# Kernel tuning notes

Measured on AMD Instinct MI355X. Metric: run time of the kernel, lower is better.

Reference implementation:

```python
import jax, jax.numpy as jnp
import numpy as np

B, N, L, H, D, IN = 512, 128, 10, 16, 8, 16
NT = B * N
E = NT * 16

def _lin(key, fan_in, shape):
    b = 1.0 / np.sqrt(fan_in)
    return jax.random.uniform(key, shape, jnp.float32, -b, b)

def setup_inputs() -> dict:
    key = jax.random.key(0)
    ks = jax.random.split(key, 12)
    x = jax.random.normal(ks[0], (NT, IN), jnp.float32)
    # within-graph random edges so to_dense_adj is well defined
    g = jax.random.randint(ks[1], (E,), 0, B)
    i = jax.random.randint(ks[2], (E,), 0, N)
    j = jax.random.randint(ks[3], (E,), 0, N)
    edge_index = jnp.stack([g * N + i, g * N + j]).astype(jnp.int32)
    return dict(
        x=x,
        gin_w1=_lin(ks[4], H, (2, L, H, H)),   # [ld/ud, layer, H, H]
        gin_b1=_lin(ks[5], H, (2, L, H)),
        gin_w2=_lin(ks[6], H, (2, L, H, H)),
        gin_b2=_lin(ks[7], H, (2, L, H)),
        mean_w=_lin(ks[8], H, (2, H, D)),
        mean_b=jnp.zeros((2, D), jnp.float32),
        std_w=_lin(ks[9], H, (2, H, D)),
        std_b=jnp.zeros((2, D), jnp.float32),
        edge_index=edge_index,
    )

def _encoder(x, w1, b1, w2, b2, mw, mb, sw, sb, src, dst):
    # PyG GIN stack: GINConv(MLP[Lin->ReLU->Lin]), eps=0, sum aggregation,
    # ReLU between layers (dropout = identity in eval mode).
    h = x
    for l in range(L):
        agg = jax.ops.segment_sum(h[src], dst, num_segments=NT)
        t = h + agg  # (1+eps)*x + sum_{j in N(i)} x_j with eps=0
        t = jnp.maximum(t @ w1[l] + b1[l], 0.0) @ w2[l] + b2[l]
        h = jnp.maximum(t, 0.0) if l < L - 1 else t
    mean = h @ mw + mb
    std = jax.nn.softplus(h @ sw + sb)
    return mean, std

def reference(x, gin_w1, gin_b1, gin_w2, gin_b2, mean_w, mean_b, std_w, std_b, edge_index):
    src, dst = edge_index[0], edge_index[1]
    enc = jax.vmap(_encoder, in_axes=(None, 0, 0, 0, 0, 0, 0, 0, 0, None, None))
    mean, std = enc(x, gin_w1, gin_b1, gin_w2, gin_b2,
                    mean_w, mean_b, std_w, std_b, src, dst)  # [2, NT, D]
    # reparameterized sample: eps ~ N(0,1) (prior.sample, detached)
    eps = jax.random.normal(jax.random.key(42), (2, NT, D), jnp.float32)
    z = mean + std * eps
    z_ld = z[0].reshape(B, N, D)
    z_ud = z[1].reshape(B, N, D)
    logits = jnp.einsum('bnd,bmd->bnm', z_ld, z_ud)  # per-graph inner-product decode
    dense_adj = jnp.zeros((B, N, N), jnp.float32).at[src // N, src % N, dst % N].add(1.0)
    n_pos = dense_adj.sum()
    posw = (B * N * N - n_pos) / n_pos
    # BCE-with-logits, pos_weight, reduction='sum'
    nll = jnp.sum(posw * dense_adj * jax.nn.softplus(-logits)
                  + (1.0 - dense_adj) * jax.nn.softplus(logits))
    # KL(N(mean,std) || N(0,1)), summed over both encoders
    kl = jnp.sum(-jnp.log(std) + 0.5 * (std * std + mean * mean) - 0.5)
    return nll, kl, jax.nn.sigmoid(logits), dense_adj
```

## Files before the change

kernel.cpp:

```cpp
#include <hip/hip_runtime.h>

#define B_    512
#define N_    128
#define L_    10
#define H_    16
#define D_    8
#define NT_   65536
#define E_    1048576
#define NNB_  8388608
#define CAP_  4096
#define CCAP_ 2816
#define HS_   20
#define PLANE_ (129*HS_ + 4)

__device__ __forceinline__ unsigned rotl32(unsigned v, int r){ return (v<<r)|(v>>(32-r)); }

__device__ __forceinline__ void threefry2x32(unsigned c0, unsigned c1, unsigned &o0, unsigned &o1){
  const unsigned ks0 = 0u, ks1 = 42u, ks2 = 0u ^ 42u ^ 0x1BD11BDAu;
  unsigned x0 = c0 + ks0, x1 = c1 + ks1;
#define TFR(r) { x0 += x1; x1 = rotl32(x1, r); x1 ^= x0; }
  TFR(13) TFR(15) TFR(26) TFR(6)   x0 += ks1; x1 += ks2 + 1u;
  TFR(17) TFR(29) TFR(16) TFR(24)  x0 += ks2; x1 += ks0 + 2u;
  TFR(13) TFR(15) TFR(26) TFR(6)   x0 += ks0; x1 += ks1 + 3u;
  TFR(17) TFR(29) TFR(16) TFR(24)  x0 += ks1; x1 += ks2 + 4u;
  TFR(13) TFR(15) TFR(26) TFR(6)   x0 += ks2; x1 += ks0 + 5u;
#undef TFR
  o0 = x0; o1 = x1;
}

__device__ __forceinline__ float erfinv_f(float x){
  float w = -log1pf(-x*x);
  float p;
  if (w < 5.0f) {
    w -= 2.5f;
    p = 2.81022636e-08f;
    p = fmaf(p, w, 3.43273939e-07f);
    p = fmaf(p, w, -3.5233877e-06f);
    p = fmaf(p, w, -4.39150654e-06f);
    p = fmaf(p, w, 0.00021858087f);
    p = fmaf(p, w, -0.00125372503f);
    p = fmaf(p, w, -0.00417768164f);
    p = fmaf(p, w, 0.246640727f);
    p = fmaf(p, w, 1.50140941f);
  } else {
    w = sqrtf(w) - 3.0f;
    p = -0.000200214257f;
    p = fmaf(p, w, 0.000100950558f);
    p = fmaf(p, w, 0.00134934322f);
    p = fmaf(p, w, -0.00367342844f);
    p = fmaf(p, w, 0.00573950773f);
    p = fmaf(p, w, -0.0076224613f);
    p = fmaf(p, w, 0.00943887047f);
    p = fmaf(p, w, 1.00167406f);
    p = fmaf(p, w, 2.83297682f);
  }
  return p * x;
}

__device__ __forceinline__ float softplus_f(float x){
  return fmaxf(x, 0.0f) + log1pf(expf(-fabsf(x)));
}

__device__ __forceinline__ void blockReduceAdd(double v, double* target){
  __shared__ double red[16];
  int lane = threadIdx.x & 63;
  int w    = threadIdx.x >> 6;
  #pragma unroll
  for(int off = 32; off > 0; off >>= 1) v += __shfl_down(v, off);
  if(lane == 0) red[w] = v;
  __syncthreads();
  if(threadIdx.x == 0){
    double s = red[0];
    int nw = (blockDim.x + 63) >> 6;
    for(int k = 1; k < nw; k++) s += red[k];
    atomicAdd(target, s);
  }
}

__device__ __forceinline__ float clamp_finite(double v){
  if(v != v) return 0.0f;
  if(v >  3.3e38) return  3.3e38f;
  if(v < -3.3e38) return -3.3e38f;
  return (float)v;
}

__global__ __launch_bounds__(1024)
void k_bin(const int* __restrict__ ei, int* __restrict__ gcount,
           unsigned short* __restrict__ ebuf){
  __shared__ int skv[4096];
  __shared__ int cnt[512];
  __shared__ int gb[512];
  __shared__ int off[512];
  __shared__ int wtot[8];
  const int t = threadIdx.x;
  if(t < 512) cnt[t] = 0;
  __syncthreads();
  int kv[4];
  const int base = blockIdx.x * 4096;
  #pragma unroll
  for(int k = 0; k < 4; k++){
    int e = base + k*1024 + t;
    int s = ei[e];
    int d = ei[E_ + e];
    int g = d >> 7;
    kv[k] = (g << 14) | ((s & 127) << 7) | (d & 127);
    atomicAdd(&cnt[g], 1);
  }
  __syncthreads();
  int intra = 0;
  if(t < 512){
    int lane = t & 63;
    int myc = cnt[t];
    int s = myc;
    #pragma unroll
    for(int o = 1; o < 64; o <<= 1){
      int v = __shfl_up(s, o);
      if(lane >= o) s += v;
    }
    intra = s - myc;
    if(lane == 63) wtot[t >> 6] = s;
    gb[t] = myc ? atomicAdd(&gcount[t], myc) : 0;
  }
  __syncthreads();
  if(t < 8){
    int v = wtot[t];
    int s = v;
    #pragma unroll
    for(int o = 1; o < 8; o <<= 1){
      int u = __shfl_up(s, o);
      if(t >= o) s += u;
    }
    wtot[t] = s - v;
  }
  if(t < 512) cnt[t] = 0;
  __syncthreads();
  if(t < 512) off[t] = intra + wtot[t >> 6];
  __syncthreads();
  #pragma unroll
  for(int k = 0; k < 4; k++){
    int g = kv[k] >> 14;
    int pos = atomicAdd(&cnt[g], 1);
    skv[off[g] + pos] = kv[k];
  }
  __syncthreads();
  #pragma unroll
  for(int k = 0; k < 4; k++){
    int i = k*1024 + t;
    int v = skv[i];
    int g = v >> 14;
    int idx = gb[g] + (i - off[g]);
    if(idx < CAP_) ebuf[(size_t)g*CAP_ + idx] = (unsigned short)(v & 0x3FFF);
  }
}

__global__ __launch_bounds__(1024, 8)
void k_mega(const float* __restrict__ x, const unsigned short* __restrict__ ebuf,
            const int* __restrict__ gcount,
            const float* __restrict__ gw1, const float* __restrict__ gb1,
            const float* __restrict__ gw2, const float* __restrict__ gb2,
            const float* __restrict__ mw,  const float* __restrict__ mb,
            const float* __restrict__ sw,  const float* __restrict__ sb,
            float* __restrict__ z, double* accb){
  __shared__ __align__(16) float hh[2*PLANE_];
  __shared__ __align__(16) float agg_l[2*128*HS_];
  __shared__ __align__(16) float u_l[2*128*HS_];
  __shared__ __align__(16) unsigned short col_l[CCAP_];
  __shared__ int off_l[129];

  const int b = blockIdx.x, t = threadIdx.x;
  const int n  = t & 127;
  const int q  = __builtin_amdgcn_readfirstlane((t >> 7) & 3);
  const int e  = __builtin_amdgcn_readfirstlane(t >> 9);
  const int q4 = q * 4;

  int* cnt = (int*)hh;

  if(t < 128) cnt[t] = 0;
  {
    uint4 s128; s128.x = s128.y = s128.z = s128.w = 0x00800080u;
    uint4* c4 = (uint4*)col_l;
    if(t < CCAP_/8) c4[t] = s128;
  }
  __syncthreads();

  int ec = gcount[b]; if(ec > CAP_) ec = CAP_;
  const unsigned short* eb = ebuf + (size_t)b*CAP_;
  for(int i = t; i < ec; i += 1024) atomicAdd(&cnt[eb[i] & 127], 1);
  __syncthreads();

  if(t < 64){
    int lane = t;
    int a0 = (cnt[lane]      + 3) & ~3;
    int a1 = (cnt[64 + lane] + 3) & ~3;
    int s0 = a0, s1 = a1;
    #pragma unroll
    for(int o = 1; o < 64; o <<= 1){
      int v0 = __shfl_up(s0, o);
      int v1 = __shfl_up(s1, o);
      if(lane >= o){ s0 += v0; s1 += v1; }
    }
    int totA = __shfl(s0, 63);
    off_l[lane]      = s0 - a0;
    off_l[64 + lane] = totA + s1 - a1;
    if(lane == 63) off_l[128] = totA + s1;
    cnt[lane] = 0; cnt[64 + lane] = 0;
  }
  __syncthreads();

  for(int i = t; i < ec; i += 1024){
    int pk = eb[i];
    int d = pk & 127;
    int pos = atomicAdd(&cnt[d], 1);
    int idx = off_l[d] + pos;
    if(idx < CCAP_) col_l[idx] = (unsigned short)(pk >> 7);
  }
  __syncthreads();
  const int r0 = off_l[n], r1 = off_l[n + 1];

  if(t < 512){
    const float4* x4 = (const float4*)x + (size_t)b*512;
    float4 v = x4[t];
    int row = t >> 2, c = (t & 3)*4;
    *(float4*)&hh[row*HS_ + c]          = v;
    *(float4*)&hh[PLANE_ + row*HS_ + c] = v;
  }
  if(t < 16){ hh[128*HS_ + t] = 0.0f; hh[PLANE_ + 128*HS_ + t] = 0.0f; }
  __syncthreads();

  const float* hb   = hh    + e*PLANE_;
  float*       aggb = agg_l + e*(128*HS_);
  float*       ub   = u_l   + e*(128*HS_);
  const float* w1g = gw1 + e*(L_*256);
  const float* w2g = gw2 + e*(L_*256);
  const float* b1g = gb1 + e*(L_*16);
  const float* b2g = gb2 + e*(L_*16);

  float hs0, hs1, hs2, hs3;
  {
    float4 s = *(const float4*)&hb[n*HS_ + q4];
    hs0 = s.x; hs1 = s.y; hs2 = s.z; hs3 = s.w;
  }

  for(int l = 0; l < L_; l++){
    float ag0 = hs0, ag1 = hs1, ag2 = hs2, ag3 = hs3;
    for(int r = r0; r < r1; r += 4){
      ushort4 c4 = *(const ushort4*)&col_l[r];
      float4 v0 = *(const float4*)&hb[c4.x*HS_ + q4];
      float4 v1 = *(const float4*)&hb[c4.y*HS_ + q4];
      float4 v2 = *(const float4*)&hb[c4.z*HS_ + q4];
      float4 v3 = *(const float4*)&hb[c4.w*HS_ + q4];
      ag0 += v0.x + v1.x + v2.x + v3.x;
      ag1 += v0.y + v1.y + v2.y + v3.y;
      ag2 += v0.z + v1.z + v2.z + v3.z;
      ag3 += v0.w + v1.w + v2.w + v3.w;
    }
    *(float4*)&aggb[n*HS_ + q4] = make_float4(ag0, ag1, ag2, ag3);
    __syncthreads();

    float av[16];
    {
      const float4* ap = (const float4*)&aggb[n*HS_];
      float4 a0 = ap[0], a1 = ap[1], a2 = ap[2], a3 = ap[3];
      av[0]=a0.x; av[1]=a0.y; av[2]=a0.z; av[3]=a0.w;
      av[4]=a1.x; av[5]=a1.y; av[6]=a1.z; av[7]=a1.w;
      av[8]=a2.x; av[9]=a2.y; av[10]=a2.z; av[11]=a2.w;
      av[12]=a3.x; av[13]=a3.y; av[14]=a3.z; av[15]=a3.w;
    }
    const float* w1c = w1g + l*256 + q4;
    float u0 = b1g[l*16 + q4 + 0];
    float u1 = b1g[l*16 + q4 + 1];
    float u2 = b1g[l*16 + q4 + 2];
    float u3 = b1g[l*16 + q4 + 3];
    #pragma unroll
    for(int k = 0; k < 16; k++){
      float a = av[k];
      const float* wr = w1c + k*16;
      u0 = fmaf(a, wr[0], u0);
      u1 = fmaf(a, wr[1], u1);
      u2 = fmaf(a, wr[2], u2);
      u3 = fmaf(a, wr[3], u3);
    }
    u0 = fmaxf(u0, 0.0f); u1 = fmaxf(u1, 0.0f);
    u2 = fmaxf(u2, 0.0f); u3 = fmaxf(u3, 0.0f);
    *(float4*)&ub[n*HS_ + q4] = make_float4(u0, u1, u2, u3);
    __syncthreads();

    float uv[16];
    {
      const float4* up = (const float4*)&ub[n*HS_];
      float4 a0 = up[0], a1 = up[1], a2 = up[2], a3 = up[3];
      uv[0]=a0.x; uv[1]=a0.y; uv[2]=a0.z; uv[3]=a0.w;
      uv[4]=a1.x; uv[5]=a1.y; uv[6]=a1.z; uv[7]=a1.w;
      uv[8]=a2.x; uv[9]=a2.y; uv[10]=a2.z; uv[11]=a2.w;
      uv[12]=a3.x; uv[13]=a3.y; uv[14]=a3.z; uv[15]=a3.w;
    }
    const float* w2c = w2g + l*256 + q4;
    float o0 = b2g[l*16 + q4 + 0];
    float o1 = b2g[l*16 + q4 + 1];
    float o2 = b2g[l*16 + q4 + 2];
    float o3 = b2g[l*16 + q4 + 3];
    #pragma unroll
    for(int k = 0; k < 16; k++){
      float a = uv[k];
      const float* wr = w2c + k*16;
      o0 = fmaf(a, wr[0], o0);
      o1 = fmaf(a, wr[1], o1);
      o2 = fmaf(a, wr[2], o2);
      o3 = fmaf(a, wr[3], o3);
    }
    if(l < L_ - 1){
      o0 = fmaxf(o0, 0.0f); o1 = fmaxf(o1, 0.0f);
      o2 = fmaxf(o2, 0.0f); o3 = fmaxf(o3, 0.0f);
    }
    hs0 = o0; hs1 = o1; hs2 = o2; hs3 = o3;
    *(float4*)&hh[e*PLANE_ + n*HS_ + q4] = make_float4(o0, o1, o2, o3);
    __syncthreads();
  }

  float hv[16];
  {
    const float4* hp = (const float4*)&hb[n*HS_];
    float4 a0 = hp[0], a1 = hp[1], a2 = hp[2], a3 = hp[3];
    hv[0]=a0.x; hv[1]=a0.y; hv[2]=a0.z; hv[3]=a0.w;
    hv[4]=a1.x; hv[5]=a1.y; hv[6]=a1.z; hv[7]=a1.w;
    hv[8]=a2.x; hv[9]=a2.y; hv[10]=a2.z; hv[11]=a2.w;
    hv[12]=a3.x; hv[13]=a3.y; hv[14]=a3.z; hv[15]=a3.w;
  }
  const float* mwg = mw + e*128; const float* mbg = mb + e*8;
  const float* swg = sw + e*128; const float* sbg = sb + e*8;
  double kll = 0.0;
  float zv[2];
  unsigned nodeBase = ((unsigned)e*NT_ + (unsigned)(b*128 + n))*8u;
  #pragma unroll
  for(int dd = 0; dd < 2; dd++){
    int d = q*2 + dd;
    float mm = mbg[d], ss = sbg[d];
    #pragma unroll
    for(int k = 0; k < 16; k++){
      mm = fmaf(hv[k], mwg[k*8 + d], mm);
      ss = fmaf(hv[k], swg[k*8 + d], ss);
    }
    float stdv = softplus_f(ss);
    unsigned o0, o1; threefry2x32(0u, nodeBase + (unsigned)d, o0, o1);
    unsigned bits = o0 ^ o1;
    float uu = __uint_as_float((bits >> 9) | 0x3f800000u) - 1.0f;
    const float lo = -0.99999994f;
    float uval = fmaxf(lo, fmaf(uu, 2.0f, lo));
    float eps = 1.41421356f * erfinv_f(uval);
    zv[dd] = mm + stdv * eps;
    float stdc = fmaxf(stdv, 1e-37f);
    float term = 0.5f*(stdv*stdv + mm*mm) - logf(stdc) - 0.5f;
    if(!(term == term) || term > 1e30f) term = 1e30f;
    kll += (double)term;
  }
  *(float2*)&z[nodeBase + (unsigned)(q*2)] = make_float2(zv[0], zv[1]);
  blockReduceAdd(kll, accb + 128 + (b & 15)*8);
}

#define TSB_ 132
#define ZUS_ 10
__global__ __launch_bounds__(1024, 2)
void k_decode(const float* __restrict__ z, const unsigned short* __restrict__ ebuf,
              const int* __restrict__ gcount, float* __restrict__ sig,
              float* __restrict__ adj, double* accb, unsigned* ticket,
              float* __restrict__ out){
  __shared__ float zl[1024];
  __shared__ float zu[128*ZUS_];
  __shared__ unsigned tile32[128*TSB_/4];
  const int b = blockIdx.x, t = threadIdx.x;
  const float* zld = z + (size_t)b*1024;
  const float* zud = z + (size_t)NT_*8 + (size_t)b*1024;
  zl[t] = zld[t];
  zu[(t >> 3)*ZUS_ + (t & 7)] = zud[t];
  for(int k = t; k < 128*TSB_/4; k += 1024) tile32[k] = 0u;
  __syncthreads();
  {
    int ec = gcount[b]; if(ec > CAP_) ec = CAP_;
    const unsigned short* eb = ebuf + (size_t)b*CAP_;
    for(int qq = t; qq < ec; qq += 1024){
      int pk = eb[qq];
      int cell = (pk >> 7)*TSB_ + (pk & 127);
      atomicAdd(&tile32[cell >> 2], 1u << ((cell & 3)*8));
    }
  }
  __syncthreads();
  const int c  = t & 127;
  const int rq = t >> 7;
  float zb[8];
  #pragma unroll
  for(int d = 0; d < 8; d++) zb[d] = zu[c*ZUS_ + d];
  float* sigb = sig + (size_t)b*16384;
  float* adjb = adj + (size_t)b*16384;
  const int sh = (c & 3)*8;
  float fl = 0.0f;
  #pragma unroll
  for(int rs = 0; rs < 16; rs++){
    int r = rq*16 + rs;
    const float* za = &zl[r*8];
    float xx = 0.0f;
    #pragma unroll
    for(int d = 0; d < 8; d++) xx = fmaf(za[d], zb[d], xx);
    unsigned packed = tile32[(r*TSB_ + c) >> 2];
    float ad = (float)((packed >> sh) & 0xFF);
    float sg = 1.0f / (1.0f + expf(-xx));
    float cc  = log1pf(expf(-fabsf(xx)));
    float spp = fmaxf(xx, 0.0f) + cc;
    float spn = fmaxf(-xx, 0.0f) + cc;
    fl += 7.0f*ad*spn + (1.0f - ad)*spp;
    sigb[r*128 + c] = sg;
    adjb[r*128 + c] = ad;
  }
  blockReduceAdd((double)fl, accb + (b & 15)*8);

  if(t == 0){
    __threadfence();
    unsigned prev = atomicAdd(ticket, 1u);
    if(prev == (unsigned)(B_ - 1)){
      double nl = 0.0, kl = 0.0;
      #pragma unroll
      for(int i = 0; i < 16; i++){
        nl += atomicAdd(&accb[i*8], 0.0);
        kl += atomicAdd(&accb[128 + i*8], 0.0);
      }
      out[0] = clamp_finite(nl);
      out[1] = clamp_finite(kl);
    }
  }
}

extern "C" void kernel_launch(void* const* d_in, const int* in_sizes, int n_in,
                              void* d_out, int out_size, void* d_ws, size_t ws_size,
                              hipStream_t stream){
  const float* x   = (const float*)d_in[0];
  const float* gw1 = (const float*)d_in[1];
  const float* gb1 = (const float*)d_in[2];
  const float* gw2 = (const float*)d_in[3];
  const float* gb2 = (const float*)d_in[4];
  const float* mw  = (const float*)d_in[5];
  const float* mb  = (const float*)d_in[6];
  const float* sw  = (const float*)d_in[7];
  const float* sb  = (const float*)d_in[8];
  const int*   ei  = (const int*)d_in[9];

  float* out = (float*)d_out;
  float* sig = out + 2;
  float* adj = out + 2 + NNB_;

  char* ws = (char*)d_ws;
  int*            gcount = (int*)(ws);
  double*         accb   = (double*)(ws + 2048);
  unsigned*       ticket = (unsigned*)(ws + 4096);
  unsigned short* ebuf   = (unsigned short*)(ws + 8192);
  float*          z      = (float*)(ws + 8192 + 2*512*CAP_);

  hipMemsetAsync(ws, 0, 8192, stream);

  k_bin   <<<E_/4096, 1024, 0, stream>>>(ei, gcount, ebuf);
  k_mega  <<<B_, 1024, 0, stream>>>(x, ebuf, gcount, gw1, gb1, gw2, gb2,
                                    mw, mb, sw, sb, z, accb);
  k_decode<<<B_, 1024, 0, stream>>>(z, ebuf, gcount, sig, adj, accb, ticket, out);
}
```

Baseline: 242.1 us.

## Fuse decode stage into encoder megakernel, keep z and adjacency tile in LDS

```diff
diff --git a/kernel.cpp b/kernel.cpp
--- a/kernel.cpp
+++ b/kernel.cpp
@@ -12,6 +12,8 @@
 #define CCAP_ 2816
 #define HS_   20
 #define PLANE_ (129*HS_ + 4)
+#define TSB_  132
+#define ZS_   12
 
 __device__ __forceinline__ unsigned rotl32(unsigned v, int r){ return (v<<r)|(v>>(32-r)); }
 
@@ -160,7 +162,8 @@
             const float* __restrict__ gw2, const float* __restrict__ gb2,
             const float* __restrict__ mw,  const float* __restrict__ mb,
             const float* __restrict__ sw,  const float* __restrict__ sb,
-            float* __restrict__ z, double* accb){
+            float* __restrict__ sig, float* __restrict__ adj,
+            double* accb, unsigned* ticket, float* __restrict__ out){
   __shared__ __align__(16) float hh[2*PLANE_];
   __shared__ __align__(16) float agg_l[2*128*HS_];
   __shared__ __align__(16) float u_l[2*128*HS_];
@@ -353,77 +356,70 @@
     if(!(term == term) || term > 1e30f) term = 1e30f;
     kll += (double)term;
   }
-  *(float2*)&z[nodeBase + (unsigned)(q*2)] = make_float2(zv[0], zv[1]);
-  blockReduceAdd(kll, accb + 128 + (b & 15)*8);
-}
-
-#define TSB_ 132
-#define ZUS_ 10
-__global__ __launch_bounds__(1024, 2)
-void k_decode(const float* __restrict__ z, const unsigned short* __restrict__ ebuf,
-              const int* __restrict__ gcount, float* __restrict__ sig,
-              float* __restrict__ adj, double* accb, unsigned* ticket,
-              float* __restrict__ out){
-  __shared__ float zl[1024];
-  __shared__ float zu[128*ZUS_];
-  __shared__ unsigned tile32[128*TSB_/4];
-  const int b = blockIdx.x, t = threadIdx.x;
-  const float* zld = z + (size_t)b*1024;
-  const float* zud = z + (size_t)NT_*8 + (size_t)b*1024;
-  zl[t] = zld[t];
-  zu[(t >> 3)*ZUS_ + (t & 7)] = zud[t];
-  for(int k = t; k < 128*TSB_/4; k += 1024) tile32[k] = 0u;
-  __syncthreads();
+
+  float*    zbuf   = u_l;
+  unsigned* tile32 = (unsigned*)agg_l;
+  *(float2*)&zbuf[e*(128*ZS_) + n*ZS_ + q*2] = make_float2(zv[0], zv[1]);
+  for(int k = t; k < 129*TSB_/4; k += 1024) tile32[k] = 0u;
+  __syncthreads();
+
+  for(int r = r0 + (t >> 7); r < r1; r += 8){
+    int src = col_l[r];
+    int cell = src*TSB_ + n;
+    atomicAdd(&tile32[cell >> 2], 1u << ((cell & 3)*8));
+  }
+  __syncthreads();
+
   {
-    int ec = gcount[b]; if(ec > CAP_) ec = CAP_;
-    const unsigned short* eb = ebuf + (size_t)b*CAP_;
-    for(int qq = t; qq < ec; qq += 1024){
-      int pk = eb[qq];
-      int cell = (pk >> 7)*TSB_ + (pk & 127);
-      atomicAdd(&tile32[cell >> 2], 1u << ((cell & 3)*8));
-    }
-  }
-  __syncthreads();
-  const int c  = t & 127;
-  const int rq = t >> 7;
-  float zb[8];
-  #pragma unroll
-  for(int d = 0; d < 8; d++) zb[d] = zu[c*ZUS_ + d];
-  float* sigb = sig + (size_t)b*16384;
-  float* adjb = adj + (size_t)b*16384;
-  const int sh = (c & 3)*8;
-  float fl = 0.0f;
-  #pragma unroll
-  for(int rs = 0; rs < 16; rs++){
-    int r = rq*16 + rs;
-    const float* za = &zl[r*8];
-    float xx = 0.0f;
-    #pragma unroll
-    for(int d = 0; d < 8; d++) xx = fmaf(za[d], zb[d], xx);
-    unsigned packed = tile32[(r*TSB_ + c) >> 2];
-    float ad = (float)((packed >> sh) & 0xFF);
-    float sg = 1.0f / (1.0f + expf(-xx));
-    float cc  = log1pf(expf(-fabsf(xx)));
-    float spp = fmaxf(xx, 0.0f) + cc;
-    float spn = fmaxf(-xx, 0.0f) + cc;
-    fl += 7.0f*ad*spn + (1.0f - ad)*spp;
-    sigb[r*128 + c] = sg;
-    adjb[r*128 + c] = ad;
-  }
-  blockReduceAdd((double)fl, accb + (b & 15)*8);
-
-  if(t == 0){
-    __threadfence();
-    unsigned prev = atomicAdd(ticket, 1u);
-    if(prev == (unsigned)(B_ - 1)){
-      double nl = 0.0, kl = 0.0;
-      #pragma unroll
-      for(int i = 0; i < 16; i++){
-        nl += atomicAdd(&accb[i*8], 0.0);
-        kl += atomicAdd(&accb[128 + i*8], 0.0);
+    const int c  = t & 127;
+    const int rq = t >> 7;
+    float zb[8];
+    {
+      float4 a = *(const float4*)&zbuf[128*ZS_ + c*ZS_];
+      float4 bq = *(const float4*)&zbuf[128*ZS_ + c*ZS_ + 4];
+      zb[0]=a.x; zb[1]=a.y; zb[2]=a.z; zb[3]=a.w;
+      zb[4]=bq.x; zb[5]=bq.y; zb[6]=bq.z; zb[7]=bq.w;
+    }
+    float* sigb = sig + (size_t)b*16384;
+    float* adjb = adj + (size_t)b*16384;
+    const int sh = (c & 3)*8;
+    float fl = 0.0f;
+    #pragma unroll
+    for(int rs = 0; rs < 16; rs++){
+      int r = rq*16 + rs;
+      float4 a0 = *(const float4*)&zbuf[r*ZS_];
+      float4 a1 = *(const float4*)&zbuf[r*ZS_ + 4];
+      float xx = a0.x*zb[0];
+      xx = fmaf(a0.y, zb[1], xx); xx = fmaf(a0.z, zb[2], xx); xx = fmaf(a0.w, zb[3], xx);
+      xx = fmaf(a1.x, zb[4], xx); xx = fmaf(a1.y, zb[5], xx);
+      xx = fmaf(a1.z, zb[6], xx); xx = fmaf(a1.w, zb[7], xx);
+      unsigned packed = tile32[(r*TSB_ + c) >> 2];
+      float ad = (float)((packed >> sh) & 0xFF);
+      float sg = 1.0f / (1.0f + expf(-xx));
+      float cc  = log1pf(expf(-fabsf(xx)));
+      float spp = fmaxf(xx, 0.0f) + cc;
+      float spn = fmaxf(-xx, 0.0f) + cc;
+      fl += 7.0f*ad*spn + (1.0f - ad)*spp;
+      sigb[r*128 + c] = sg;
+      adjb[r*128 + c] = ad;
+    }
+
+    blockReduceAdd(kll, accb + 128 + (b & 15)*8);
+    __syncthreads();
+    blockReduceAdd((double)fl, accb + (b & 15)*8);
+    if(t == 0){
+      __threadfence();
+      unsigned prev = atomicAdd(ticket, 1u);
+      if(prev == (unsigned)(B_ - 1)){
+        double nl = 0.0, kl = 0.0;
+        #pragma unroll
+        for(int i = 0; i < 16; i++){
+          nl += atomicAdd(&accb[i*8], 0.0);
+          kl += atomicAdd(&accb[128 + i*8], 0.0);
+        }
+        out[0] = clamp_finite(nl);
+        out[1] = clamp_finite(kl);
       }
-      out[0] = clamp_finite(nl);
-      out[1] = clamp_finite(kl);
     }
   }
 }
@@ -451,12 +447,10 @@
   double*         accb   = (double*)(ws + 2048);
   unsigned*       ticket = (unsigned*)(ws + 4096);
   unsigned short* ebuf   = (unsigned short*)(ws + 8192);
-  float*          z      = (float*)(ws + 8192 + 2*512*CAP_);
 
   hipMemsetAsync(ws, 0, 8192, stream);
 
-  k_bin   <<<E_/4096, 1024, 0, stream>>>(ei, gcount, ebuf);
-  k_mega  <<<B_, 1024, 0, stream>>>(x, ebuf, gcount, gw1, gb1, gw2, gb2,
-                                    mw, mb, sw, sb, z, accb);
-  k_decode<<<B_, 1024, 0, stream>>>(z, ebuf, gcount, sig, adj, accb, ticket, out);
-}
+  k_bin  <<<E_/4096, 1024, 0, stream>>>(ei, gcount, ebuf);
+  k_mega <<<B_, 1024, 0, stream>>>(x, ebuf, gcount, gw1, gb1, gw2, gb2,
+                                   mw, mb, sw, sb, sig, adj, accb, ticket, out);
+}
```

Result: no change. 240.1 us (-0.8%).
